# Kernel tuning notes

Measured on AMD Instinct MI355X. Metric: run time of the kernel, lower is better.

## Reference

```python
import jax, jax.numpy as jnp
import numpy as np

EMBED_DIM = 1024
HIDDEN = 128
N_QUERY = 65536
N_PROTO = 512


def setup_inputs() -> dict:
    key = jax.random.key(0)
    k1, k2, k3, k4, k5, k6, k7 = jax.random.split(key, 7)
    d2 = EMBED_DIM * 2
    lim1 = 1.0 / np.sqrt(d2)
    lim2 = 1.0 / np.sqrt(HIDDEN)
    return {
        "query_features": jax.random.normal(k1, (N_QUERY, EMBED_DIM), dtype=jnp.float32),
        "prototypes": jax.random.normal(k2, (N_PROTO, EMBED_DIM), dtype=jnp.float32),
        "distances": jax.random.uniform(k3, (N_QUERY, N_PROTO), dtype=jnp.float32),
        "W1": jax.random.uniform(k4, (d2, HIDDEN), minval=-lim1, maxval=lim1, dtype=jnp.float32),
        "b1": jax.random.uniform(k5, (HIDDEN,), minval=-lim1, maxval=lim1, dtype=jnp.float32),
        "W2": jax.random.uniform(k6, (HIDDEN, 1), minval=-lim2, maxval=lim2, dtype=jnp.float32),
        "b2": jax.random.uniform(k7, (1,), minval=-lim2, maxval=lim2, dtype=jnp.float32),
    }


def reference(query_features, prototypes, distances, W1, b1, W2, b2):
    # Batched version of the per-query loop: argmin -> gather -> concat -> MLP.
    idx = jnp.argmin(distances, axis=1)                      # [N_QUERY]
    closest = prototypes[idx]                                # [N_QUERY, D]
    combined = jnp.concatenate([query_features, closest], axis=-1)  # [N_QUERY, 2D]
    h = jax.nn.relu(combined @ W1 + b1)                      # [N_QUERY, 128]
    out = jax.nn.sigmoid(h @ W2 + b2)                        # [N_QUERY, 1]
    return jnp.squeeze(out, axis=-1)                         # [N_QUERY]
```

## Files before the change

### kernel.cpp

```cpp
#include <hip/hip_runtime.h>
#include <hip/hip_bf16.h>
#include <math.h>

#define EMBED 1024
#define HIDDEN 128
#define NPROTO 512
#define LDA 72

typedef short bf16x8 __attribute__((ext_vector_type(8)));
typedef float f32x4 __attribute__((ext_vector_type(4)));

__device__ __forceinline__ unsigned short f2bf(float x) {
    unsigned u = __builtin_bit_cast(unsigned, x);
    unsigned r = u + 0x7FFFu + ((u >> 16) & 1u);
    return (unsigned short)(r >> 16);
}

__global__ __launch_bounds__(256) void prep_kernel(
    const float* __restrict__ prototypes,
    const float* __restrict__ W1,
    float* __restrict__ proto_h,
    unsigned short* __restrict__ w1t)
{
    int b = blockIdx.x;
    int t = threadIdx.x;
    if (b < 256) {
        int ph = t >> 7, h = t & 127;
        int p = b * 2 + ph;
        const float* pr = prototypes + (size_t)p * EMBED;
        const float* w  = W1 + (size_t)EMBED * HIDDEN + h;
        float acc = 0.f;
        for (int k = 0; k < EMBED; k += 8) {
            #pragma unroll
            for (int j = 0; j < 8; ++j)
                acc += pr[k + j] * w[(size_t)(k + j) * HIDDEN];
        }
        proto_h[(size_t)p * HIDDEN + h] = acc;
    } else {
        int s = (b - 256) * 256 + t;
        int n = s & 127;
        int k0 = (s >> 7) * 8;
        bf16x8 v;
        #pragma unroll
        for (int j = 0; j < 8; ++j)
            v[j] = (short)f2bf(W1[(size_t)(k0 + j) * HIDDEN + n]);
        *(bf16x8*)(w1t + (size_t)n * EMBED + k0) = v;
    }
}

__global__ __launch_bounds__(256, 3) void main_kernel(
    const float* __restrict__ qf,
    const float* __restrict__ dist,
    const float* __restrict__ b1,
    const float* __restrict__ W2,
    const float* __restrict__ b2,
    const float* __restrict__ proto_h,
    const unsigned short* __restrict__ w1t,
    float* __restrict__ out)
{
    __shared__ unsigned short a_lds[2][128 * LDA];
    __shared__ int s_idx[128];
    __shared__ float s_red[128][2];

    int t = threadIdx.x;
    int wave = t >> 6, lane = t & 63;
    int q0 = blockIdx.x * 128;

    int sm = t >> 3;
    int sk = (t & 7) * 8;

    float4 pre[4][2];
    {
        const float* base = qf + (size_t)q0 * EMBED;
        #pragma unroll
        for (int i = 0; i < 4; ++i) {
            const float* src = base + (size_t)(sm + i * 32) * EMBED + sk;
            pre[i][0] = *(const float4*)src;
            pre[i][1] = *(const float4*)(src + 4);
        }
    }

    for (int i = 0; i < 32; i += 4) {
        float4 v0[4], v1[4];
        #pragma unroll
        for (int j = 0; j < 4; ++j) {
            const float* dr = dist + (size_t)(q0 + wave * 32 + i + j) * NPROTO;
            v0[j] = ((const float4*)dr)[lane];
            v1[j] = ((const float4*)dr)[lane + 64];
        }
        #pragma unroll
        for (int j = 0; j < 4; ++j) {
            float bv = v0[j].x; int bi = lane * 4;
            if (v0[j].y < bv) { bv = v0[j].y; bi = lane * 4 + 1; }
            if (v0[j].z < bv) { bv = v0[j].z; bi = lane * 4 + 2; }
            if (v0[j].w < bv) { bv = v0[j].w; bi = lane * 4 + 3; }
            int c = 256 + lane * 4;
            if (v1[j].x < bv) { bv = v1[j].x; bi = c; }
            if (v1[j].y < bv) { bv = v1[j].y; bi = c + 1; }
            if (v1[j].z < bv) { bv = v1[j].z; bi = c + 2; }
            if (v1[j].w < bv) { bv = v1[j].w; bi = c + 3; }
            #pragma unroll
            for (int s = 1; s < 64; s <<= 1) {
                float ov = __shfl_xor(bv, s);
                int   oi = __shfl_xor(bi, s);
                if (ov < bv || (ov == bv && oi < bi)) { bv = ov; bi = oi; }
            }
            if (lane == 0) s_idx[wave * 32 + i + j] = bi;
        }
    }

    #pragma unroll
    for (int i = 0; i < 4; ++i) {
        bf16x8 pk;
        pk[0] = (short)f2bf(pre[i][0].x); pk[1] = (short)f2bf(pre[i][0].y);
        pk[2] = (short)f2bf(pre[i][0].z); pk[3] = (short)f2bf(pre[i][0].w);
        pk[4] = (short)f2bf(pre[i][1].x); pk[5] = (short)f2bf(pre[i][1].y);
        pk[6] = (short)f2bf(pre[i][1].z); pk[7] = (short)f2bf(pre[i][1].w);
        *(bf16x8*)(&a_lds[0][(sm + i * 32) * LDA + sk]) = pk;
    }
    __syncthreads();

    int wave_m = wave >> 1, wave_n = wave & 1;
    int quad = lane >> 4, tid16 = lane & 15;
    f32x4 acc[4][4];
    #pragma unroll
    for (int mi = 0; mi < 4; ++mi)
        #pragma unroll
        for (int ni = 0; ni < 4; ++ni)
            acc[mi][ni] = (f32x4){0.f, 0.f, 0.f, 0.f};

    for (int kt = 0; kt < EMBED; kt += 64) {
        int cur = (kt >> 6) & 1;
        bool more = (kt + 64) < EMBED;

        bf16x8 bfr[2][4];
        #pragma unroll
        for (int ks = 0; ks < 2; ++ks)
            #pragma unroll
            for (int ni = 0; ni < 4; ++ni)
                bfr[ks][ni] = *(const bf16x8*)(
                    w1t + (size_t)(wave_n * 64 + ni * 16 + tid16) * EMBED
                        + kt + ks * 32 + quad * 8);

        if (more) {
            const float* base = qf + (size_t)q0 * EMBED + kt + 64;
            #pragma unroll
            for (int i = 0; i < 4; ++i) {
                const float* src = base + (size_t)(sm + i * 32) * EMBED + sk;
                pre[i][0] = *(const float4*)src;
                pre[i][1] = *(const float4*)(src + 4);
            }
        }

        #pragma unroll
        for (int ks = 0; ks < 2; ++ks) {
            int kk = ks * 32 + quad * 8;
            bf16x8 af[4];
            #pragma unroll
            for (int mi = 0; mi < 4; ++mi)
                af[mi] = *(bf16x8*)(&a_lds[cur][(wave_m * 64 + mi * 16 + tid16) * LDA + kk]);
            #pragma unroll
            for (int mi = 0; mi < 4; ++mi)
                #pragma unroll
                for (int ni = 0; ni < 4; ++ni)
                    acc[mi][ni] = __builtin_amdgcn_mfma_f32_16x16x32_bf16(
                        af[mi], bfr[ks][ni], acc[mi][ni], 0, 0, 0);
        }

        if (more) {
            #pragma unroll
            for (int i = 0; i < 4; ++i) {
                bf16x8 pk;
                pk[0] = (short)f2bf(pre[i][0].x); pk[1] = (short)f2bf(pre[i][0].y);
                pk[2] = (short)f2bf(pre[i][0].z); pk[3] = (short)f2bf(pre[i][0].w);
                pk[4] = (short)f2bf(pre[i][1].x); pk[5] = (short)f2bf(pre[i][1].y);
                pk[6] = (short)f2bf(pre[i][1].z); pk[7] = (short)f2bf(pre[i][1].w);
                *(bf16x8*)(&a_lds[cur ^ 1][(sm + i * 32) * LDA + sk]) = pk;
            }
        }
        __syncthreads();
    }

    float b1v[4], w2v[4];
    #pragma unroll
    for (int ni = 0; ni < 4; ++ni) {
        int n = wave_n * 64 + ni * 16 + tid16;
        b1v[ni] = b1[n];
        w2v[ni] = W2[n];
    }
    #pragma unroll
    for (int mi = 0; mi < 4; ++mi) {
        #pragma unroll
        for (int r = 0; r < 4; ++r) {
            int m = wave_m * 64 + mi * 16 + quad * 4 + r;
            const float* ph = proto_h + (size_t)s_idx[m] * HIDDEN;
            float sum = 0.f;
            #pragma unroll
            for (int ni = 0; ni < 4; ++ni) {
                int n = wave_n * 64 + ni * 16 + tid16;
                float v = acc[mi][ni][r] + b1v[ni] + ph[n];
                sum += fmaxf(v, 0.f) * w2v[ni];
            }
            #pragma unroll
            for (int s = 1; s < 16; s <<= 1) sum += __shfl_xor(sum, s);
            if (tid16 == 0) s_red[m][wave_n] = sum;
        }
    }
    __syncthreads();
    if (t < 128) {
        float s = s_red[t][0] + s_red[t][1] + b2[0];
        out[q0 + t] = 1.f / (1.f + expf(-s));
    }
}

extern "C" void kernel_launch(void* const* d_in, const int* in_sizes, int n_in,
                              void* d_out, int out_size, void* d_ws, size_t ws_size,
                              hipStream_t stream) {
    const float* qf    = (const float*)d_in[0];
    const float* proto = (const float*)d_in[1];
    const float* dist  = (const float*)d_in[2];
    const float* W1    = (const float*)d_in[3];
    const float* b1    = (const float*)d_in[4];
    const float* W2    = (const float*)d_in[5];
    const float* b2    = (const float*)d_in[6];
    float* out = (float*)d_out;

    float* proto_h = (float*)d_ws;
    unsigned short* w1t = (unsigned short*)((char*)d_ws + 512 * 128 * 4);

    prep_kernel<<<320, 256, 0, stream>>>(proto, W1, proto_h, w1t);

    int nq = in_sizes[0] / EMBED;
    main_kernel<<<nq / 128, 256, 0, stream>>>(qf, dist, b1, W2, b2, proto_h, w1t, out);
}
```

Measured before the change: 504.1 us.

## Load query rows straight into MFMA registers and drop the LDS staging

Rewrites the GEMM so each wave owns 16 query rows and all 128 hidden columns. A fragments are loaded from global memory straight into registers and converted to bf16, replacing the double-buffered LDS tiles and the per-iteration barriers. The block tile shrinks to 64 queries, occupancy is raised to 4 blocks, and bf16 packing moves to a cheaper round-half-up conversion. In exchange, W1 fragments are now reloaded by every wave with no cross-wave reuse, and the query loads are strided and less coalesced. The rounding also changes slightly from round-to-nearest-even.

```diff
diff --git a/kernel.cpp b/kernel.cpp
--- a/kernel.cpp
+++ b/kernel.cpp
@@ -5,15 +5,27 @@
 #define EMBED 1024
 #define HIDDEN 128
 #define NPROTO 512
-#define LDA 72
 
 typedef short bf16x8 __attribute__((ext_vector_type(8)));
-typedef float f32x4 __attribute__((ext_vector_type(4)));
+typedef int   i32x4  __attribute__((ext_vector_type(4)));
+typedef float f32x4  __attribute__((ext_vector_type(4)));
 
 __device__ __forceinline__ unsigned short f2bf(float x) {
     unsigned u = __builtin_bit_cast(unsigned, x);
     unsigned r = u + 0x7FFFu + ((u >> 16) & 1u);
     return (unsigned short)(r >> 16);
+}
+
+__device__ __forceinline__ unsigned pack_bf2(float x, float y) {
+    unsigned ux = __builtin_bit_cast(unsigned, x) + 0x8000u;
+    unsigned uy = __builtin_bit_cast(unsigned, y) + 0x8000u;
+    return (uy & 0xFFFF0000u) | (ux >> 16);
+}
+__device__ __forceinline__ bf16x8 pack_bf8(float4 a, float4 b) {
+    i32x4 r;
+    r.x = (int)pack_bf2(a.x, a.y); r.y = (int)pack_bf2(a.z, a.w);
+    r.z = (int)pack_bf2(b.x, b.y); r.w = (int)pack_bf2(b.z, b.w);
+    return __builtin_bit_cast(bf16x8, r);
 }
 
 __global__ __launch_bounds__(256) void prep_kernel(
@@ -48,7 +60,7 @@
     }
 }
 
-__global__ __launch_bounds__(256, 3) void main_kernel(
+__global__ __launch_bounds__(256, 4) void main_kernel(
     const float* __restrict__ qf,
     const float* __restrict__ dist,
     const float* __restrict__ b1,
@@ -58,33 +70,18 @@
     const unsigned short* __restrict__ w1t,
     float* __restrict__ out)
 {
-    __shared__ unsigned short a_lds[2][128 * LDA];
-    __shared__ int s_idx[128];
-    __shared__ float s_red[128][2];
+    __shared__ int s_idx[64];
 
     int t = threadIdx.x;
     int wave = t >> 6, lane = t & 63;
-    int q0 = blockIdx.x * 128;
+    int quad = lane >> 4, tid16 = lane & 15;
+    int q0 = blockIdx.x * 64;
 
-    int sm = t >> 3;
-    int sk = (t & 7) * 8;
-
-    float4 pre[4][2];
-    {
-        const float* base = qf + (size_t)q0 * EMBED;
-        #pragma unroll
-        for (int i = 0; i < 4; ++i) {
-            const float* src = base + (size_t)(sm + i * 32) * EMBED + sk;
-            pre[i][0] = *(const float4*)src;
-            pre[i][1] = *(const float4*)(src + 4);
-        }
-    }
-
-    for (int i = 0; i < 32; i += 4) {
+    for (int i = 0; i < 16; i += 4) {
         float4 v0[4], v1[4];
         #pragma unroll
         for (int j = 0; j < 4; ++j) {
-            const float* dr = dist + (size_t)(q0 + wave * 32 + i + j) * NPROTO;
+            const float* dr = dist + (size_t)(q0 + wave * 16 + i + j) * NPROTO;
             v0[j] = ((const float4*)dr)[lane];
             v1[j] = ((const float4*)dr)[lane + 64];
         }
@@ -105,111 +102,64 @@
                 int   oi = __shfl_xor(bi, s);
                 if (ov < bv || (ov == bv && oi < bi)) { bv = ov; bi = oi; }
             }
-            if (lane == 0) s_idx[wave * 32 + i + j] = bi;
+            if (lane == 0) s_idx[wave * 16 + i + j] = bi;
         }
-    }
-
-    #pragma unroll
-    for (int i = 0; i < 4; ++i) {
-        bf16x8 pk;
-        pk[0] = (short)f2bf(pre[i][0].x); pk[1] = (short)f2bf(pre[i][0].y);
-        pk[2] = (short)f2bf(pre[i][0].z); pk[3] = (short)f2bf(pre[i][0].w);
-        pk[4] = (short)f2bf(pre[i][1].x); pk[5] = (short)f2bf(pre[i][1].y);
-        pk[6] = (short)f2bf(pre[i][1].z); pk[7] = (short)f2bf(pre[i][1].w);
-        *(bf16x8*)(&a_lds[0][(sm + i * 32) * LDA + sk]) = pk;
     }
     __syncthreads();
 
-    int wave_m = wave >> 1, wave_n = wave & 1;
-    int quad = lane >> 4, tid16 = lane & 15;
-    f32x4 acc[4][4];
+    f32x4 acc[8];
     #pragma unroll
-    for (int mi = 0; mi < 4; ++mi)
-        #pragma unroll
-        for (int ni = 0; ni < 4; ++ni)
-            acc[mi][ni] = (f32x4){0.f, 0.f, 0.f, 0.f};
+    for (int ni = 0; ni < 8; ++ni) acc[ni] = (f32x4){0.f, 0.f, 0.f, 0.f};
+
+    const float* abase = qf + (size_t)(q0 + wave * 16 + tid16) * EMBED + quad * 8;
+    const unsigned short* bbase = w1t + (size_t)tid16 * EMBED + quad * 8;
 
     for (int kt = 0; kt < EMBED; kt += 64) {
-        int cur = (kt >> 6) & 1;
-        bool more = (kt + 64) < EMBED;
+        float4 a0 = *(const float4*)(abase + kt);
+        float4 a1 = *(const float4*)(abase + kt + 4);
+        float4 a2 = *(const float4*)(abase + kt + 32);
+        float4 a3 = *(const float4*)(abase + kt + 36);
 
-        bf16x8 bfr[2][4];
+        bf16x8 bfr[8];
         #pragma unroll
-        for (int ks = 0; ks < 2; ++ks)
-            #pragma unroll
-            for (int ni = 0; ni < 4; ++ni)
-                bfr[ks][ni] = *(const bf16x8*)(
-                    w1t + (size_t)(wave_n * 64 + ni * 16 + tid16) * EMBED
-                        + kt + ks * 32 + quad * 8);
-
-        if (more) {
-            const float* base = qf + (size_t)q0 * EMBED + kt + 64;
-            #pragma unroll
-            for (int i = 0; i < 4; ++i) {
-                const float* src = base + (size_t)(sm + i * 32) * EMBED + sk;
-                pre[i][0] = *(const float4*)src;
-                pre[i][1] = *(const float4*)(src + 4);
-            }
-        }
+        for (int ni = 0; ni < 8; ++ni)
+            bfr[ni] = *(const bf16x8*)(bbase + (size_t)(ni * 16) * EMBED + kt);
+        bf16x8 af0 = pack_bf8(a0, a1);
+        #pragma unroll
+        for (int ni = 0; ni < 8; ++ni)
+            acc[ni] = __builtin_amdgcn_mfma_f32_16x16x32_bf16(af0, bfr[ni], acc[ni], 0, 0, 0);
 
         #pragma unroll
-        for (int ks = 0; ks < 2; ++ks) {
-            int kk = ks * 32 + quad * 8;
-            bf16x8 af[4];
-            #pragma unroll
-            for (int mi = 0; mi < 4; ++mi)
-                af[mi] = *(bf16x8*)(&a_lds[cur][(wave_m * 64 + mi * 16 + tid16) * LDA + kk]);
-            #pragma unroll
-            for (int mi = 0; mi < 4; ++mi)
-                #pragma unroll
-                for (int ni = 0; ni < 4; ++ni)
-                    acc[mi][ni] = __builtin_amdgcn_mfma_f32_16x16x32_bf16(
-                        af[mi], bfr[ks][ni], acc[mi][ni], 0, 0, 0);
-        }
-
-        if (more) {
-            #pragma unroll
-            for (int i = 0; i < 4; ++i) {
-                bf16x8 pk;
-                pk[0] = (short)f2bf(pre[i][0].x); pk[1] = (short)f2bf(pre[i][0].y);
-                pk[2] = (short)f2bf(pre[i][0].z); pk[3] = (short)f2bf(pre[i][0].w);
-                pk[4] = (short)f2bf(pre[i][1].x); pk[5] = (short)f2bf(pre[i][1].y);
-                pk[6] = (short)f2bf(pre[i][1].z); pk[7] = (short)f2bf(pre[i][1].w);
-                *(bf16x8*)(&a_lds[cur ^ 1][(sm + i * 32) * LDA + sk]) = pk;
-            }
-        }
-        __syncthreads();
+        for (int ni = 0; ni < 8; ++ni)
+            bfr[ni] = *(const bf16x8*)(bbase + (size_t)(ni * 16) * EMBED + kt + 32);
+        bf16x8 af1 = pack_bf8(a2, a3);
+        #pragma unroll
+        for (int ni = 0; ni < 8; ++ni)
+            acc[ni] = __builtin_amdgcn_mfma_f32_16x16x32_bf16(af1, bfr[ni], acc[ni], 0, 0, 0);
     }
 
-    float b1v[4], w2v[4];
+    float b1v[8], w2v[8];
     #pragma unroll
-    for (int ni = 0; ni < 4; ++ni) {
-        int n = wave_n * 64 + ni * 16 + tid16;
+    for (int ni = 0; ni < 8; ++ni) {
+        int n = ni * 16 + tid16;
         b1v[ni] = b1[n];
         w2v[ni] = W2[n];
     }
+    float bias2 = b2[0];
     #pragma unroll
-    for (int mi = 0; mi < 4; ++mi) {
+    for (int r = 0; r < 4; ++r) {
+        int row = wave * 16 + quad * 4 + r;
+        const float* ph = proto_h + (size_t)s_idx[row] * HIDDEN;
+        float sum = 0.f;
         #pragma unroll
-        for (int r = 0; r < 4; ++r) {
-            int m = wave_m * 64 + mi * 16 + quad * 4 + r;
-            const float* ph = proto_h + (size_t)s_idx[m] * HIDDEN;
-            float sum = 0.f;
-            #pragma unroll
-            for (int ni = 0; ni < 4; ++ni) {
-                int n = wave_n * 64 + ni * 16 + tid16;
-                float v = acc[mi][ni][r] + b1v[ni] + ph[n];
-                sum += fmaxf(v, 0.f) * w2v[ni];
-            }
-            #pragma unroll
-            for (int s = 1; s < 16; s <<= 1) sum += __shfl_xor(sum, s);
-            if (tid16 == 0) s_red[m][wave_n] = sum;
+        for (int ni = 0; ni < 8; ++ni) {
+            float v = acc[ni][r] + b1v[ni] + ph[ni * 16 + tid16];
+            sum += fmaxf(v, 0.f) * w2v[ni];
         }
-    }
-    __syncthreads();
-    if (t < 128) {
-        float s = s_red[t][0] + s_red[t][1] + b2[0];
-        out[q0 + t] = 1.f / (1.f + expf(-s));
+        #pragma unroll
+        for (int s = 1; s < 16; s <<= 1) sum += __shfl_xor(sum, s);
+        if (tid16 == 0)
+            out[q0 + row] = 1.f / (1.f + expf(-(sum + bias2)));
     }
 }
 
@@ -231,5 +181,5 @@
     prep_kernel<<<320, 256, 0, stream>>>(proto, W1, proto_h, w1t);
 
     int nq = in_sizes[0] / EMBED;
-    main_kernel<<<nq / 128, 256, 0, stream>>>(qf, dist, b1, W2, b2, proto_h, w1t, out);
+    main_kernel<<<nq / 64, 256, 0, stream>>>(qf, dist, b1, W2, b2, proto_h, w1t, out);
 }
```

Measured after the change: 553.4 us. +9.8%, slower.
